# Kernel optimization log

Hardware: AMD Instinct MI355X
Metric: run time of the kernel (lower is better)

## Reference

```python
import jax, jax.numpy as jnp
import numpy as np

B, S, D = 2, 2048, 2048
NH, NKV, HD = 16, 4, 128
NREP = NH // NKV
EPS = 1e-6
ROPE_THETA = 1e6


def _rms_norm(x, w, eps=EPS):
    # normalize over last dim (head_dim)
    var = jnp.mean(x * x, axis=-1, keepdims=True)
    return x * jax.lax.rsqrt(var + eps) * w


def _rotate_half(x):
    x1, x2 = jnp.split(x, 2, axis=-1)
    return jnp.concatenate((-x2, x1), axis=-1)


def setup_inputs() -> dict:
    key = jax.random.key(0)
    ks = jax.random.split(key, 7)
    x = jax.random.normal(ks[0], (B, S, D), dtype=jnp.float32)
    # RoPE cache: [S, 2*HD] = concat(cos, sin), NeoX-style (freqs duplicated)
    pos = jnp.arange(S, dtype=jnp.float32)
    inv_freq = 1.0 / (ROPE_THETA ** (jnp.arange(0, HD, 2, dtype=jnp.float32) / HD))
    freqs = pos[:, None] * inv_freq[None, :]          # [S, HD//2]
    emb = jnp.concatenate((freqs, freqs), axis=-1)    # [S, HD]
    rope_cache = jnp.concatenate((jnp.cos(emb), jnp.sin(emb)), axis=-1)  # [S, 2*HD]
    wq = jax.random.normal(ks[1], (NH * HD, D), dtype=jnp.float32) * 0.02
    wk = jax.random.normal(ks[2], (NKV * HD, D), dtype=jnp.float32) * 0.02
    wv = jax.random.normal(ks[3], (NKV * HD, D), dtype=jnp.float32) * 0.02
    wo = jax.random.normal(ks[4], (D, NH * HD), dtype=jnp.float32) * 0.02
    q_norm_w = jnp.ones((HD,), dtype=jnp.float32)
    k_norm_w = jnp.ones((HD,), dtype=jnp.float32)
    return {"x": x, "rope_cache": rope_cache, "wq": wq, "wk": wk,
            "wv": wv, "wo": wo, "q_norm_w": q_norm_w, "k_norm_w": k_norm_w}


def reference(x, rope_cache, wq, wk, wv, wo, q_norm_w, k_norm_w):
    bs, seqlen, _ = x.shape
    scale = HD ** -0.5
    # QKV projections (no bias)
    xq = (x @ wq.T).reshape(bs, seqlen, NH, HD)
    xk = (x @ wk.T).reshape(bs, seqlen, NKV, HD)
    xv = (x @ wv.T).reshape(bs, seqlen, NKV, HD)
    # q/k RMSNorm over head_dim
    xq = _rms_norm(xq, q_norm_w)
    xk = _rms_norm(xk, k_norm_w)
    # RoPE: rope_cache[:S] -> cos [1,S,1,HD], sin [1,S,1,HD]
    rc = rope_cache[:seqlen].reshape(1, seqlen, 1, 2 * HD)
    cos, sin = rc[..., :HD], rc[..., HD:]
    xq = xq * cos + _rotate_half(xq) * sin
    xk = xk * cos + _rotate_half(xk) * sin
    # GQA attention without materializing repeated KV heads:
    # q: [b,s,NKV,NREP,HD]; k,v: [b,s,NKV,HD]
    q = xq.reshape(bs, seqlen, NKV, NREP, HD)
    scores = jnp.einsum('bqgrd,bkgd->bgrqk', q, xk) * scale
    causal = jnp.tril(jnp.ones((seqlen, seqlen), dtype=bool))
    scores = jnp.where(causal, scores, jnp.finfo(scores.dtype).min)
    probs = jax.nn.softmax(scores, axis=-1)
    out = jnp.einsum('bgrqk,bkgd->bqgrd', probs, xv)
    out = out.reshape(bs, seqlen, NH * HD)
    return out @ wo.T
```

## Files before the change

kernel.cpp:

```cpp
#include <hip/hip_runtime.h>
#include <hip/hip_bf16.h>
#include <stdint.h>

typedef float f32x4 __attribute__((ext_vector_type(4)));
typedef __bf16 bf16x8 __attribute__((ext_vector_type(8)));
typedef unsigned short u16x4 __attribute__((ext_vector_type(4)));

#define DEV __device__ __forceinline__
#define NEG_BIG (-3.0e38f)

DEV f32x4 mfma16(bf16x8 a, bf16x8 b, f32x4 c) {
  return __builtin_amdgcn_mfma_f32_16x16x32_bf16(a, b, c, 0, 0, 0);
}

DEV void gl_lds16(const void* g, void* l) {
  __builtin_amdgcn_global_load_lds(
      (const __attribute__((address_space(1))) void*)g,
      (__attribute__((address_space(3))) void*)l,
      16, 0, 0);
}

DEV void wait_vm0() {
  asm volatile("s_waitcnt vmcnt(0)" ::: "memory");
  __builtin_amdgcn_sched_barrier(0);
}

DEV unsigned short f2bfu(float f) {
  __hip_bfloat16 h = __float2bfloat16(f);
  return __builtin_bit_cast(unsigned short, h);
}

__global__ __launch_bounds__(256) void cvt_f32_bf16(
    const float* __restrict__ src, __hip_bfloat16* __restrict__ dst, int n4)
{
  const int i = blockIdx.x * 256 + threadIdx.x;
  if (i >= n4) return;
  const float4 v = ((const float4*)src)[i];
  u16x4 o;
  o[0] = f2bfu(v.x); o[1] = f2bfu(v.y); o[2] = f2bfu(v.z); o[3] = f2bfu(v.w);
  ((u16x4*)dst)[i] = o;
}

DEV void storeC(__hip_bfloat16* C, size_t idx, float v) { C[idx] = __float2bfloat16(v); }
DEV void storeC(float* C, size_t idx, float v) { C[idx] = v; }

template <typename OutT, bool TRANS>
__global__ __launch_bounds__(256) void gemm_bt(
    const __hip_bfloat16* __restrict__ A,
    const __hip_bfloat16* __restrict__ B,
    OutT* __restrict__ C,
    int M, int N, int K, int ldc)
{
  __shared__ __align__(16) unsigned short ldsA[2][128 * 32];
  __shared__ __align__(16) unsigned short ldsB[2][128 * 32];

  const int tid  = threadIdx.x;
  const int w    = tid >> 6;
  const int lane = tid & 63;
  const int mbase = blockIdx.y * 128;
  const int nbase = blockIdx.x * 128;
  const int wr = (w >> 1) * 64;
  const int wc = (w & 1) * 64;

  const int srow = tid >> 2;
  const int scol = (tid & 3) * 8;
  const __hip_bfloat16* Ag = A + (size_t)(mbase + srow) * K + scol;
  const __hip_bfloat16* Bg = B + (size_t)(nbase + srow) * K + scol;

  f32x4 acc[4][4] = {};

  const int KT = K >> 5;
  int cur = 0;

  #pragma unroll
  for (int i = 0; i < 2; ++i) {
    gl_lds16(Ag + (size_t)i * 64 * K, &ldsA[0][i * 2048 + w * 512]);
    gl_lds16(Bg + (size_t)i * 64 * K, &ldsB[0][i * 2048 + w * 512]);
  }
  wait_vm0();
  __syncthreads();

  const int arow = wr + (lane & 15);
  const int brow = wc + (lane & 15);
  const int koff = (lane >> 4) * 8;

  for (int kt = 0; kt < KT; ++kt) {
    if (kt + 1 < KT) {
      const int k0 = (kt + 1) << 5;
      #pragma unroll
      for (int i = 0; i < 2; ++i) {
        gl_lds16(Ag + (size_t)i * 64 * K + k0, &ldsA[cur ^ 1][i * 2048 + w * 512]);
        gl_lds16(Bg + (size_t)i * 64 * K + k0, &ldsB[cur ^ 1][i * 2048 + w * 512]);
      }
    }
    bf16x8 af[4], bfr[4];
    #pragma unroll
    for (int mi = 0; mi < 4; ++mi)
      af[mi] = *(const bf16x8*)&ldsA[cur][(arow + mi * 16) * 32 + koff];
    #pragma unroll
    for (int ni = 0; ni < 4; ++ni)
      bfr[ni] = *(const bf16x8*)&ldsB[cur][(brow + ni * 16) * 32 + koff];
    #pragma unroll
    for (int mi = 0; mi < 4; ++mi)
      #pragma unroll
      for (int ni = 0; ni < 4; ++ni)
        acc[mi][ni] = mfma16(af[mi], bfr[ni], acc[mi][ni]);
    wait_vm0();
    __syncthreads();
    cur ^= 1;
  }

  #pragma unroll
  for (int mi = 0; mi < 4; ++mi)
    #pragma unroll
    for (int ni = 0; ni < 4; ++ni)
      #pragma unroll
      for (int j = 0; j < 4; ++j) {
        const int m = mbase + wr + mi * 16 + (lane >> 4) * 4 + j;
        const int n = nbase + wc + ni * 16 + (lane & 15);
        if (TRANS) storeC(C, (size_t)n * ldc + m, acc[mi][ni][j]);
        else       storeC(C, (size_t)m * ldc + n, acc[mi][ni][j]);
      }
}

__global__ __launch_bounds__(256) void rmsnorm_rope(
    __hip_bfloat16* __restrict__ qk,
    const float* __restrict__ rope,
    const float* __restrict__ qw,
    const float* __restrict__ kw)
{
  const int v = blockIdx.x * 4 + (threadIdx.x >> 6);
  const int lane = threadIdx.x & 63;
  const int row = v / 20;
  const int hh  = v % 20;
  const int s   = row & 2047;

  __hip_bfloat16* p = qk + (size_t)row * 2560 +
                      (hh < 16 ? hh * 128 : 2048 + (hh - 16) * 128);
  const float* wn = (hh < 16) ? qw : kw;

  float x0 = __bfloat162float(p[lane]);
  float x1 = __bfloat162float(p[lane + 64]);
  float ss = x0 * x0 + x1 * x1;
  #pragma unroll
  for (int off = 1; off < 64; off <<= 1) ss += __shfl_xor(ss, off);
  const float rn = rsqrtf(ss * (1.0f / 128.0f) + 1e-6f);
  x0 *= rn * wn[lane];
  x1 *= rn * wn[lane + 64];

  const float* rc = rope + (size_t)s * 256;
  p[lane]      = __float2bfloat16(x0 * rc[lane]      - x1 * rc[128 + lane]);
  p[lane + 64] = __float2bfloat16(x1 * rc[64 + lane] + x0 * rc[192 + lane]);
}

struct AttnState {
  f32x4 po[8];
  float mrow[4];
  float lrow[4];
};

DEV void attn_tile(const unsigned short* K_, const unsigned short* V_,
                   unsigned short* P_, const bf16x8* qf, AttnState& st_,
                   int kv0, int q0, int qmaxw, int lane)
{
  if (kv0 > qmaxw) return;
  const int l15 = lane & 15, lg = lane >> 4;

  f32x4 st[2];
  #pragma unroll
  for (int sub = 0; sub < 2; ++sub) {
    f32x4 s = {};
    const int kvloc = sub * 16 + l15;
    #pragma unroll
    for (int dt = 0; dt < 4; ++dt) {
      const int slot = (dt * 4 + lg) ^ (kvloc & 7);
      bf16x8 kf = *(const bf16x8*)&K_[kvloc * 128 + slot * 8];
      s = mfma16(qf[dt], kf, s);
    }
    st[sub] = s;
  }
  #pragma unroll
  for (int sub = 0; sub < 2; ++sub)
    #pragma unroll
    for (int j = 0; j < 4; ++j) {
      const float val = st[sub][j] * 0.08838834764831845f;
      const int kv = kv0 + sub * 16 + l15;
      st[sub][j] = (kv > q0 + j) ? NEG_BIG : val;
    }
  float pm[4];
  #pragma unroll
  for (int j = 0; j < 4; ++j) pm[j] = fmaxf(st[0][j], st[1][j]);
  #pragma unroll
  for (int off = 1; off < 16; off <<= 1)
    #pragma unroll
    for (int j = 0; j < 4; ++j) pm[j] = fmaxf(pm[j], __shfl_xor(pm[j], off));
  float corr[4];
  #pragma unroll
  for (int j = 0; j < 4; ++j) {
    const float mn = fmaxf(st_.mrow[j], pm[j]);
    corr[j] = __expf(st_.mrow[j] - mn);
    st_.mrow[j] = mn;
  }
  float rs[4] = {0.f, 0.f, 0.f, 0.f};
  #pragma unroll
  for (int sub = 0; sub < 2; ++sub)
    #pragma unroll
    for (int j = 0; j < 4; ++j) {
      const float pv = __expf(st[sub][j] - st_.mrow[j]);
      st[sub][j] = pv;
      rs[j] += pv;
    }
  #pragma unroll
  for (int off = 1; off < 16; off <<= 1)
    #pragma unroll
    for (int j = 0; j < 4; ++j) rs[j] += __shfl_xor(rs[j], off);
  #pragma unroll
  for (int j = 0; j < 4; ++j) st_.lrow[j] = st_.lrow[j] * corr[j] + rs[j];
  #pragma unroll
  for (int dt = 0; dt < 8; ++dt)
    #pragma unroll
    for (int j = 0; j < 4; ++j) st_.po[dt][j] *= corr[j];

  #pragma unroll
  for (int sub = 0; sub < 2; ++sub)
    #pragma unroll
    for (int j = 0; j < 4; ++j)
      P_[(lg * 4 + j) * 40 + sub * 16 + l15] = f2bfu(st[sub][j]);
  asm volatile("s_waitcnt lgkmcnt(0)" ::: "memory");
  __builtin_amdgcn_sched_barrier(0);
  bf16x8 pf = *(const bf16x8*)&P_[l15 * 40 + lg * 8];

  #pragma unroll
  for (int dt = 0; dt < 8; ++dt) {
    const int d = dt * 16 + l15;
    bf16x8 vf = *(const bf16x8*)&V_[d * 32 + ((lg ^ (l15 >> 2)) * 8)];
    st_.po[dt] = mfma16(pf, vf, st_.po[dt]);
  }
}

__global__ __launch_bounds__(256) void attn_fwd(
    const __hip_bfloat16* __restrict__ qk,
    const __hip_bfloat16* __restrict__ VT,
    __hip_bfloat16* __restrict__ O)
{
  __shared__ __align__(16) unsigned short ldsK[2][32 * 128];
  __shared__ __align__(16) unsigned short ldsV[2][128 * 32];
  __shared__ __align__(16) unsigned short ldsP[4][16 * 40];

  const int tid  = threadIdx.x;
  const int w    = tid >> 6;
  const int lane = tid & 63;
  const int qtA = blockIdx.x;
  const int qtB = 31 - qtA;
  const int h  = blockIdx.y;
  const int b  = blockIdx.z;
  const int hkv = h >> 2;

  const size_t LDQ = 2560;
  const __hip_bfloat16* Qb = qk + (size_t)b * 2048 * LDQ + h * 128;
  const __hip_bfloat16* Kb = qk + (size_t)b * 2048 * LDQ + 2048 + hkv * 128;
  const __hip_bfloat16* Vb = VT + (size_t)(hkv * 128) * 4096 + b * 2048;

  const int krow = tid >> 4;
  const int kcol = ((tid & 15) ^ (krow & 7)) * 8;
  const int vdrow = tid >> 2;
  const int vs8 = ((tid & 3) ^ ((tid >> 4) & 3)) * 8;

  const int l15 = lane & 15;
  const int koff = (lane >> 4) * 8;

  bf16x8 qfA[4], qfB[4];
  {
    const int qrA = qtA * 64 + w * 16 + l15;
    const int qrB = qtB * 64 + w * 16 + l15;
    #pragma unroll
    for (int dt = 0; dt < 4; ++dt) {
      qfA[dt] = *(const bf16x8*)(Qb + (size_t)qrA * LDQ + dt * 32 + koff);
      qfB[dt] = *(const bf16x8*)(Qb + (size_t)qrB * LDQ + dt * 32 + koff);
    }
  }

  const int ntA = 2 * qtA + 2;
  const int T   = 66;

#define STAGE(kv0_, buf_) do { \
    _Pragma("unroll") \
    for (int i = 0; i < 2; ++i) \
      gl_lds16(Kb + (size_t)((kv0_) + i * 16 + krow) * LDQ + kcol, \
               &ldsK[buf_][i * 2048 + w * 512]); \
    _Pragma("unroll") \
    for (int i = 0; i < 2; ++i) \
      gl_lds16(Vb + (size_t)(i * 64 + vdrow) * 4096 + (kv0_) + vs8, \
               &ldsV[buf_][i * 2048 + w * 512]); \
  } while (0)

  STAGE(0, 0);
  wait_vm0();
  __syncthreads();

  {
    AttnState st_;
    #pragma unroll
    for (int dt = 0; dt < 8; ++dt) st_.po[dt] = f32x4{};
    #pragma unroll
    for (int j = 0; j < 4; ++j) { st_.mrow[j] = NEG_BIG; st_.lrow[j] = 0.f; }
    const int q0 = qtA * 64 + w * 16 + (lane >> 4) * 4;
    const int qm = qtA * 64 + w * 16 + 15;
    for (int t = 0; t < ntA; ++t) {
      const int nx = t + 1;
      const int nkv0 = (nx < ntA ? nx : nx - ntA) * 32;
      STAGE(nkv0, nx & 1);
      attn_tile(ldsK[t & 1], ldsV[t & 1], ldsP[w], qfA, st_, t * 32, q0, qm, lane);
      wait_vm0();
      __syncthreads();
    }
    #pragma unroll
    for (int j = 0; j < 4; ++j) {
      const float inv = 1.0f / st_.lrow[j];
      const int q = q0 + j;
      #pragma unroll
      for (int dt = 0; dt < 8; ++dt)
        O[((size_t)b * 2048 + q) * 2048 + h * 128 + dt * 16 + l15] =
            __float2bfloat16(st_.po[dt][j] * inv);
    }
  }

  {
    AttnState st_;
    #pragma unroll
    for (int dt = 0; dt < 8; ++dt) st_.po[dt] = f32x4{};
    #pragma unroll
    for (int j = 0; j < 4; ++j) { st_.mrow[j] = NEG_BIG; st_.lrow[j] = 0.f; }
    const int q0 = qtB * 64 + w * 16 + (lane >> 4) * 4;
    const int qm = qtB * 64 + w * 16 + 15;
    for (int t = ntA; t < T; ++t) {
      const int nx = t + 1;
      if (nx < T) STAGE((nx - ntA) * 32, nx & 1);
      attn_tile(ldsK[t & 1], ldsV[t & 1], ldsP[w], qfB, st_, (t - ntA) * 32, q0, qm, lane);
      wait_vm0();
      __syncthreads();
    }
    #pragma unroll
    for (int j = 0; j < 4; ++j) {
      const float inv = 1.0f / st_.lrow[j];
      const int q = q0 + j;
      #pragma unroll
      for (int dt = 0; dt < 8; ++dt)
        O[((size_t)b * 2048 + q) * 2048 + h * 128 + dt * 16 + l15] =
            __float2bfloat16(st_.po[dt][j] * inv);
    }
  }
#undef STAGE
}

extern "C" void kernel_launch(void* const* d_in, const int* in_sizes, int n_in,
                              void* d_out, int out_size, void* d_ws, size_t ws_size,
                              hipStream_t stream) {
  (void)in_sizes; (void)n_in; (void)out_size; (void)ws_size;
  const float* x    = (const float*)d_in[0];
  const float* rope = (const float*)d_in[1];
  const float* wq   = (const float*)d_in[2];
  const float* wk   = (const float*)d_in[3];
  const float* wv   = (const float*)d_in[4];
  const float* wo   = (const float*)d_in[5];
  const float* qnw  = (const float*)d_in[6];
  const float* knw  = (const float*)d_in[7];
  float* out = (float*)d_out;

  __hip_bfloat16* xb  = (__hip_bfloat16*)d_ws;
  __hip_bfloat16* wb  = xb  + (size_t)4096 * 2048;
  __hip_bfloat16* wob = wb  + (size_t)3072 * 2048;
  __hip_bfloat16* qkb = wob + (size_t)2048 * 2048;
  __hip_bfloat16* vt  = qkb + (size_t)4096 * 2560;
  __hip_bfloat16* att = vt  + (size_t)512 * 4096;

  cvt_f32_bf16<<<8192, 256, 0, stream>>>(x,  xb,  2097152);
  cvt_f32_bf16<<<4096, 256, 0, stream>>>(wq, wb,                     1048576);
  cvt_f32_bf16<<<1024, 256, 0, stream>>>(wk, wb + (size_t)2048*2048,  262144);
  cvt_f32_bf16<<<1024, 256, 0, stream>>>(wv, wb + (size_t)2560*2048,  262144);
  cvt_f32_bf16<<<4096, 256, 0, stream>>>(wo, wob,                    1048576);

  gemm_bt<__hip_bfloat16, false><<<dim3(20, 32), 256, 0, stream>>>(
      xb, wb, qkb, 4096, 2560, 2048, 2560);
  gemm_bt<__hip_bfloat16, true><<<dim3(4, 32), 256, 0, stream>>>(
      xb, wb + (size_t)2560 * 2048, vt, 4096, 512, 2048, 4096);
  rmsnorm_rope<<<20480, 256, 0, stream>>>(qkb, rope, qnw, knw);
  attn_fwd<<<dim3(16, 16, 2), 256, 0, stream>>>(qkb, vt, att);
  gemm_bt<float, false><<<dim3(16, 32), 256, 0, stream>>>(
      att, wob, out, 4096, 2048, 2048, 2048);
}
```

Baseline: 422.0 us.

## Widen attention KV tiles to 64, fold scale into Q, lazy rescale, fuse conversions

Attention now processes 64-key tiles instead of 32, with larger LDS buffers and a new V swizzle, halving loop iterations and barriers. The softmax scale times log2(e) is folded into Q during the RMSNorm/RoPE pass, so the attention loop uses exp2f with no per-score multiply. The running-max rescale of the accumulator is skipped unless the max grows by more than a threshold, and causal masking is applied only on diagonal tiles. The five fp32-to-bf16 conversion launches are merged into one kernel; the lazy rescale and the larger LDS footprint carry some numerical and occupancy risk.

Measured after the change: 382.5 us. 9.3% less time.

```diff
diff --git a/kernel.cpp b/kernel.cpp
--- a/kernel.cpp
+++ b/kernel.cpp
@@ -8,6 +8,7 @@
 
 #define DEV __device__ __forceinline__
 #define NEG_BIG (-3.0e38f)
+#define QSCALE_LOG2E 0.12751744532f
 
 DEV f32x4 mfma16(bf16x8 a, bf16x8 b, f32x4 c) {
   return __builtin_amdgcn_mfma_f32_16x16x32_bf16(a, b, c, 0, 0, 0);
@@ -30,15 +31,24 @@
   return __builtin_bit_cast(unsigned short, h);
 }
 
-__global__ __launch_bounds__(256) void cvt_f32_bf16(
-    const float* __restrict__ src, __hip_bfloat16* __restrict__ dst, int n4)
+__global__ __launch_bounds__(256) void cvt_all(
+    const float* __restrict__ x,  const float* __restrict__ wq,
+    const float* __restrict__ wk, const float* __restrict__ wv,
+    const float* __restrict__ wo,
+    __hip_bfloat16* __restrict__ xb, __hip_bfloat16* __restrict__ wb,
+    __hip_bfloat16* __restrict__ wob)
 {
-  const int i = blockIdx.x * 256 + threadIdx.x;
-  if (i >= n4) return;
-  const float4 v = ((const float4*)src)[i];
+  int i = blockIdx.x * 256 + threadIdx.x;
+  const float* s; __hip_bfloat16* d;
+  if (i < 2097152)      { s = x;  d = xb; }
+  else if (i < 3145728) { s = wq; d = wb;                        i -= 2097152; }
+  else if (i < 3407872) { s = wk; d = wb + (size_t)2048 * 2048;  i -= 3145728; }
+  else if (i < 3670016) { s = wv; d = wb + (size_t)2560 * 2048;  i -= 3407872; }
+  else                  { s = wo; d = wob;                       i -= 3670016; }
+  const float4 v = ((const float4*)s)[i];
   u16x4 o;
   o[0] = f2bfu(v.x); o[1] = f2bfu(v.y); o[2] = f2bfu(v.z); o[3] = f2bfu(v.w);
-  ((u16x4*)dst)[i] = o;
+  ((u16x4*)d)[i] = o;
 }
 
 DEV void storeC(__hip_bfloat16* C, size_t idx, float v) { C[idx] = __float2bfloat16(v); }
@@ -138,6 +148,7 @@
   __hip_bfloat16* p = qk + (size_t)row * 2560 +
                       (hh < 16 ? hh * 128 : 2048 + (hh - 16) * 128);
   const float* wn = (hh < 16) ? qw : kw;
+  const float os = (hh < 16) ? QSCALE_LOG2E : 1.0f;
 
   float x0 = __bfloat162float(p[lane]);
   float x1 = __bfloat162float(p[lane + 64]);
@@ -149,8 +160,8 @@
   x1 *= rn * wn[lane + 64];
 
   const float* rc = rope + (size_t)s * 256;
-  p[lane]      = __float2bfloat16(x0 * rc[lane]      - x1 * rc[128 + lane]);
-  p[lane + 64] = __float2bfloat16(x1 * rc[64 + lane] + x0 * rc[192 + lane]);
+  p[lane]      = __float2bfloat16((x0 * rc[lane]      - x1 * rc[128 + lane]) * os);
+  p[lane + 64] = __float2bfloat16((x1 * rc[64 + lane] + x0 * rc[192 + lane]) * os);
 }
 
 struct AttnState {
@@ -161,14 +172,13 @@
 
 DEV void attn_tile(const unsigned short* K_, const unsigned short* V_,
                    unsigned short* P_, const bf16x8* qf, AttnState& st_,
-                   int kv0, int q0, int qmaxw, int lane)
+                   int kv0, int q0, int qminw, int lane)
 {
-  if (kv0 > qmaxw) return;
   const int l15 = lane & 15, lg = lane >> 4;
 
-  f32x4 st[2];
-  #pragma unroll
-  for (int sub = 0; sub < 2; ++sub) {
+  f32x4 st[4];
+  #pragma unroll
+  for (int sub = 0; sub < 4; ++sub) {
     f32x4 s = {};
     const int kvloc = sub * 16 + l15;
     #pragma unroll
@@ -179,34 +189,43 @@
     }
     st[sub] = s;
   }
-  #pragma unroll
-  for (int sub = 0; sub < 2; ++sub)
+  if (kv0 + 63 > qminw) {
+    #pragma unroll
+    for (int sub = 0; sub < 4; ++sub)
+      #pragma unroll
+      for (int j = 0; j < 4; ++j) {
+        const int kv = kv0 + sub * 16 + l15;
+        if (kv > q0 + j) st[sub][j] = NEG_BIG;
+      }
+  }
+  float pm[4];
+  #pragma unroll
+  for (int j = 0; j < 4; ++j)
+    pm[j] = fmaxf(fmaxf(st[0][j], st[1][j]), fmaxf(st[2][j], st[3][j]));
+  #pragma unroll
+  for (int off = 1; off < 16; off <<= 1)
+    #pragma unroll
+    for (int j = 0; j < 4; ++j) pm[j] = fmaxf(pm[j], __shfl_xor(pm[j], off));
+  bool need = false;
+  #pragma unroll
+  for (int j = 0; j < 4; ++j) need = need || (pm[j] > st_.mrow[j] + 8.f);
+  if (__any(need)) {
     #pragma unroll
     for (int j = 0; j < 4; ++j) {
-      const float val = st[sub][j] * 0.08838834764831845f;
-      const int kv = kv0 + sub * 16 + l15;
-      st[sub][j] = (kv > q0 + j) ? NEG_BIG : val;
-    }
-  float pm[4];
-  #pragma unroll
-  for (int j = 0; j < 4; ++j) pm[j] = fmaxf(st[0][j], st[1][j]);
-  #pragma unroll
-  for (int off = 1; off < 16; off <<= 1)
-    #pragma unroll
-    for (int j = 0; j < 4; ++j) pm[j] = fmaxf(pm[j], __shfl_xor(pm[j], off));
-  float corr[4];
-  #pragma unroll
-  for (int j = 0; j < 4; ++j) {
-    const float mn = fmaxf(st_.mrow[j], pm[j]);
-    corr[j] = __expf(st_.mrow[j] - mn);
-    st_.mrow[j] = mn;
+      const float mn = fmaxf(st_.mrow[j], pm[j]);
+      const float corr = exp2f(st_.mrow[j] - mn);
+      st_.mrow[j] = mn;
+      st_.lrow[j] *= corr;
+      #pragma unroll
+      for (int dt = 0; dt < 8; ++dt) st_.po[dt][j] *= corr;
+    }
   }
   float rs[4] = {0.f, 0.f, 0.f, 0.f};
   #pragma unroll
-  for (int sub = 0; sub < 2; ++sub)
+  for (int sub = 0; sub < 4; ++sub)
     #pragma unroll
     for (int j = 0; j < 4; ++j) {
-      const float pv = __expf(st[sub][j] - st_.mrow[j]);
+      const float pv = exp2f(st[sub][j] - st_.mrow[j]);
       st[sub][j] = pv;
       rs[j] += pv;
     }
@@ -215,26 +234,25 @@
     #pragma unroll
     for (int j = 0; j < 4; ++j) rs[j] += __shfl_xor(rs[j], off);
   #pragma unroll
-  for (int j = 0; j < 4; ++j) st_.lrow[j] = st_.lrow[j] * corr[j] + rs[j];
-  #pragma unroll
-  for (int dt = 0; dt < 8; ++dt)
-    #pragma unroll
-    for (int j = 0; j < 4; ++j) st_.po[dt][j] *= corr[j];
-
-  #pragma unroll
-  for (int sub = 0; sub < 2; ++sub)
+  for (int j = 0; j < 4; ++j) st_.lrow[j] += rs[j];
+
+  #pragma unroll
+  for (int sub = 0; sub < 4; ++sub)
     #pragma unroll
     for (int j = 0; j < 4; ++j)
-      P_[(lg * 4 + j) * 40 + sub * 16 + l15] = f2bfu(st[sub][j]);
+      P_[(lg * 4 + j) * 72 + sub * 16 + l15] = f2bfu(st[sub][j]);
   asm volatile("s_waitcnt lgkmcnt(0)" ::: "memory");
   __builtin_amdgcn_sched_barrier(0);
-  bf16x8 pf = *(const bf16x8*)&P_[l15 * 40 + lg * 8];
+  bf16x8 pf0 = *(const bf16x8*)&P_[l15 * 72 + lg * 8];
+  bf16x8 pf1 = *(const bf16x8*)&P_[l15 * 72 + 32 + lg * 8];
 
   #pragma unroll
   for (int dt = 0; dt < 8; ++dt) {
     const int d = dt * 16 + l15;
-    bf16x8 vf = *(const bf16x8*)&V_[d * 32 + ((lg ^ (l15 >> 2)) * 8)];
-    st_.po[dt] = mfma16(pf, vf, st_.po[dt]);
+    bf16x8 v0 = *(const bf16x8*)&V_[d * 64 + ((lg       ^ (d & 7))) * 8];
+    bf16x8 v1 = *(const bf16x8*)&V_[d * 64 + (((4 + lg) ^ (d & 7))) * 8];
+    st_.po[dt] = mfma16(pf0, v0, st_.po[dt]);
+    st_.po[dt] = mfma16(pf1, v1, st_.po[dt]);
   }
 }
 
@@ -243,9 +261,9 @@
     const __hip_bfloat16* __restrict__ VT,
     __hip_bfloat16* __restrict__ O)
 {
-  __shared__ __align__(16) unsigned short ldsK[2][32 * 128];
-  __shared__ __align__(16) unsigned short ldsV[2][128 * 32];
-  __shared__ __align__(16) unsigned short ldsP[4][16 * 40];
+  __shared__ __align__(16) unsigned short ldsK[2][64 * 128];
+  __shared__ __align__(16) unsigned short ldsV[2][128 * 64];
+  __shared__ __align__(16) unsigned short ldsP[4][16 * 72];
 
   const int tid  = threadIdx.x;
   const int w    = tid >> 6;
@@ -263,8 +281,8 @@
 
   const int krow = tid >> 4;
   const int kcol = ((tid & 15) ^ (krow & 7)) * 8;
-  const int vdrow = tid >> 2;
-  const int vs8 = ((tid & 3) ^ ((tid >> 4) & 3)) * 8;
+  const int vdrow = tid >> 3;
+  const int vs8 = ((tid & 7) ^ (vdrow & 7)) * 8;
 
   const int l15 = lane & 15;
   const int koff = (lane >> 4) * 8;
@@ -280,17 +298,17 @@
     }
   }
 
-  const int ntA = 2 * qtA + 2;
-  const int T   = 66;
+  const int ntA = qtA + 1;
+  const int T   = 33;
 
 #define STAGE(kv0_, buf_) do { \
     _Pragma("unroll") \
-    for (int i = 0; i < 2; ++i) \
+    for (int i = 0; i < 4; ++i) \
       gl_lds16(Kb + (size_t)((kv0_) + i * 16 + krow) * LDQ + kcol, \
                &ldsK[buf_][i * 2048 + w * 512]); \
     _Pragma("unroll") \
-    for (int i = 0; i < 2; ++i) \
-      gl_lds16(Vb + (size_t)(i * 64 + vdrow) * 4096 + (kv0_) + vs8, \
+    for (int i = 0; i < 4; ++i) \
+      gl_lds16(Vb + (size_t)(i * 32 + vdrow) * 4096 + (kv0_) + vs8, \
                &ldsV[buf_][i * 2048 + w * 512]); \
   } while (0)
 
@@ -305,12 +323,12 @@
     #pragma unroll
     for (int j = 0; j < 4; ++j) { st_.mrow[j] = NEG_BIG; st_.lrow[j] = 0.f; }
     const int q0 = qtA * 64 + w * 16 + (lane >> 4) * 4;
-    const int qm = qtA * 64 + w * 16 + 15;
+    const int qminw = qtA * 64 + w * 16;
     for (int t = 0; t < ntA; ++t) {
       const int nx = t + 1;
-      const int nkv0 = (nx < ntA ? nx : nx - ntA) * 32;
+      const int nkv0 = (nx < ntA ? nx : nx - ntA) * 64;
       STAGE(nkv0, nx & 1);
-      attn_tile(ldsK[t & 1], ldsV[t & 1], ldsP[w], qfA, st_, t * 32, q0, qm, lane);
+      attn_tile(ldsK[t & 1], ldsV[t & 1], ldsP[w], qfA, st_, t * 64, q0, qminw, lane);
       wait_vm0();
       __syncthreads();
     }
@@ -332,11 +350,11 @@
     #pragma unroll
     for (int j = 0; j < 4; ++j) { st_.mrow[j] = NEG_BIG; st_.lrow[j] = 0.f; }
     const int q0 = qtB * 64 + w * 16 + (lane >> 4) * 4;
-    const int qm = qtB * 64 + w * 16 + 15;
+    const int qminw = qtB * 64 + w * 16;
     for (int t = ntA; t < T; ++t) {
       const int nx = t + 1;
-      if (nx < T) STAGE((nx - ntA) * 32, nx & 1);
-      attn_tile(ldsK[t & 1], ldsV[t & 1], ldsP[w], qfB, st_, (t - ntA) * 32, q0, qm, lane);
+      if (nx < T) STAGE((nx - ntA) * 64, nx & 1);
+      attn_tile(ldsK[t & 1], ldsV[t & 1], ldsP[w], qfB, st_, (t - ntA) * 64, q0, qminw, lane);
       wait_vm0();
       __syncthreads();
     }
@@ -374,11 +392,7 @@
   __hip_bfloat16* vt  = qkb + (size_t)4096 * 2560;
   __hip_bfloat16* att = vt  + (size_t)512 * 4096;
 
-  cvt_f32_bf16<<<8192, 256, 0, stream>>>(x,  xb,  2097152);
-  cvt_f32_bf16<<<4096, 256, 0, stream>>>(wq, wb,                     1048576);
-  cvt_f32_bf16<<<1024, 256, 0, stream>>>(wk, wb + (size_t)2048*2048,  262144);
-  cvt_f32_bf16<<<1024, 256, 0, stream>>>(wv, wb + (size_t)2560*2048,  262144);
-  cvt_f32_bf16<<<4096, 256, 0, stream>>>(wo, wob,                    1048576);
+  cvt_all<<<18432, 256, 0, stream>>>(x, wq, wk, wv, wo, xb, wb, wob);
 
   gemm_bt<__hip_bfloat16, false><<<dim3(20, 32), 256, 0, stream>>>(
       xb, wb, qkb, 4096, 2560, 2048, 2560);
```
